# Optimization experiments

Hardware: AMD Instinct MI355X
Metric: run time of the kernel (lower is better)

Reference implementation:

```python
import jax, jax.numpy as jnp
import numpy as np

H = 8       # heads
D = 512     # hidden_size
DH = D // H # head dim
FF = 2048   # hardcoded FFN hidden in source


def _layernorm(x, g, b, eps=1e-5):
    mu = jnp.mean(x, axis=-1, keepdims=True)
    var = jnp.var(x, axis=-1, keepdims=True)
    return (x - mu) * jax.lax.rsqrt(var + eps) * g + b


def setup_inputs() -> dict:
    key = jax.random.key(0)
    ks = jax.random.split(key, 12)
    B, S = 2, 4096
    s = lambda fan_in: 1.0 / np.sqrt(fan_in)
    return {
        "reaction": jax.random.normal(ks[0], (B, S, D), dtype=jnp.float32),
        "mask": jnp.ones((B, 1, 1, S), dtype=jnp.int32),
        # attention weights stored as [in, out] (torch Linear weight.T)
        "Wq": jax.random.uniform(ks[1], (D, D), jnp.float32, -s(D), s(D)),
        "Wk": jax.random.uniform(ks[2], (D, D), jnp.float32, -s(D), s(D)),
        "Wv": jax.random.uniform(ks[3], (D, D), jnp.float32, -s(D), s(D)),
        "Wo": jax.random.uniform(ks[4], (D, D), jnp.float32, -s(D), s(D)),
        "bo": jnp.zeros((D,), jnp.float32),
        "W1": jax.random.uniform(ks[5], (D, FF), jnp.float32, -s(D), s(D)),
        "b1": jnp.zeros((FF,), jnp.float32),
        "W2": jax.random.uniform(ks[6], (FF, D), jnp.float32, -s(FF), s(FF)),
        "b2": jnp.zeros((D,), jnp.float32),
        "g_sa": jnp.ones((D,), jnp.float32),
        "b_sa": jnp.zeros((D,), jnp.float32),
        "g_ff": jnp.ones((D,), jnp.float32),
        "b_ff": jnp.zeros((D,), jnp.float32),
    }


def reference(reaction, mask, Wq, Wk, Wv, Wo, bo, W1, b1, W2, b2, g_sa, b_sa, g_ff, b_ff):
    B, S, _ = reaction.shape
    # --- self-attention part (pre-norm) ---
    x = _layernorm(reaction, g_sa, b_sa)
    q = (x @ Wq).reshape(B, S, H, DH)
    k = (x @ Wk).reshape(B, S, H, DH)
    v = (x @ Wv).reshape(B, S, H, DH)
    scale = DH ** (-0.5)
    scores = jnp.einsum('bqhd,bkhd->bhqk', q * scale, k)  # [B,H,S,S]
    scores = jnp.where(mask == 0, -jnp.inf, scores)
    att = jax.nn.softmax(scores, axis=-1)
    ctx = jnp.einsum('bhqk,bkhd->bqhd', att, v).reshape(B, S, D)
    attn_out = jax.nn.gelu(ctx @ Wo + bo, approximate=False)  # GELU after output proj (as in source)
    x = attn_out + reaction
    # --- feed-forward part (pre-norm) ---
    y = _layernorm(x, g_ff, b_ff)
    y = jax.nn.gelu(y @ W1 + b1, approximate=False) @ W2 + b2
    return y + x
```

## Files before the change

### kernel.cpp

```cpp
#include <hip/hip_runtime.h>
#include <hip/hip_bf16.h>
#include <math.h>

#define HN 8
#define DM 512
#define DHD 64
#define FFD 2048
#define BB 2
#define SS 4096
#define MT (BB*SS)

typedef __bf16 bf16_t;
typedef __bf16 bf16x8 __attribute__((ext_vector_type(8)));
typedef __bf16 bf16x4 __attribute__((ext_vector_type(4)));
typedef float  floatx4 __attribute__((ext_vector_type(4)));

__device__ __forceinline__ void async_copy16(const bf16_t* g, bf16_t* l) {
  __builtin_amdgcn_global_load_lds((const __attribute__((address_space(1))) void*)g,
                                   (__attribute__((address_space(3))) void*)l,
                                   16, 0, 0);
}

#if __has_builtin(__builtin_amdgcn_exp2f)
__device__ __forceinline__ float fast_exp2(float x) { return __builtin_amdgcn_exp2f(x); }
#else
__device__ __forceinline__ float fast_exp2(float x) { return __expf(x * 0.69314718056f); }
#endif

__device__ __forceinline__ float gelu_f(float x) {
  float y = 0.7978845608f * (x + 0.044715f * x * x * x);
  float e = fast_exp2(y * 2.885390082f);
  float th = 1.0f - 2.0f / (e + 1.0f);
  return 0.5f * x * (1.0f + th);
}

__global__ __launch_bounds__(256)
void ln_kernel(const float* __restrict__ x, const float* __restrict__ g,
               const float* __restrict__ be, bf16_t* __restrict__ out)
{
  const int wave = threadIdx.x >> 6, lane = threadIdx.x & 63;
  const int row = blockIdx.x * 4 + wave;
  const float* xr = x + (size_t)row * DM + lane * 8;
  float4 a = *(const float4*)xr;
  float4 c = *(const float4*)(xr + 4);
  float s  = (a.x + a.y) + (a.z + a.w) + (c.x + c.y) + (c.z + c.w);
  float s2 = (a.x*a.x + a.y*a.y) + (a.z*a.z + a.w*a.w)
           + (c.x*c.x + c.y*c.y) + (c.z*c.z + c.w*c.w);
#pragma unroll
  for (int o = 1; o < 64; o <<= 1) { s += __shfl_xor(s, o); s2 += __shfl_xor(s2, o); }
  const float mu = s * (1.0f / DM);
  const float rv = rsqrtf(s2 * (1.0f / DM) - mu * mu + 1e-5f);
  float4 g0 = *(const float4*)(g + lane * 8);
  float4 g1 = *(const float4*)(g + lane * 8 + 4);
  float4 b0 = *(const float4*)(be + lane * 8);
  float4 b1 = *(const float4*)(be + lane * 8 + 4);
  bf16x8 o8;
  o8[0] = (bf16_t)((a.x - mu) * rv * g0.x + b0.x);
  o8[1] = (bf16_t)((a.y - mu) * rv * g0.y + b0.y);
  o8[2] = (bf16_t)((a.z - mu) * rv * g0.z + b0.z);
  o8[3] = (bf16_t)((a.w - mu) * rv * g0.w + b0.w);
  o8[4] = (bf16_t)((c.x - mu) * rv * g1.x + b1.x);
  o8[5] = (bf16_t)((c.y - mu) * rv * g1.y + b1.y);
  o8[6] = (bf16_t)((c.z - mu) * rv * g1.z + b1.z);
  o8[7] = (bf16_t)((c.w - mu) * rv * g1.w + b1.w);
  *(bf16x8*)(out + (size_t)row * DM + lane * 8) = o8;
}

__global__ __launch_bounds__(256)
void prep_weights(const float* __restrict__ Wq, const float* __restrict__ Wk,
                  const float* __restrict__ Wv, const float* __restrict__ Wo,
                  const float* __restrict__ W1, const float* __restrict__ W2,
                  bf16_t* __restrict__ WqkvT, bf16_t* __restrict__ WoT,
                  bf16_t* __restrict__ W1T, bf16_t* __restrict__ W2T)
{
  const int bid = blockIdx.x;
  const float* src; bf16_t* dst; int Kd, Nd, n0, k0;
  if (bid < 768) {
    int seg = bid >> 8, t = bid & 255;
    src = (seg == 0) ? Wq : (seg == 1) ? Wk : Wv;
    dst = WqkvT + (size_t)seg * 512 * 512;
    Kd = 512; Nd = 512; n0 = (t & 15) * 32; k0 = (t >> 4) * 32;
  } else if (bid < 1024) {
    int t = bid - 768; src = Wo; dst = WoT;
    Kd = 512; Nd = 512; n0 = (t & 15) * 32; k0 = (t >> 4) * 32;
  } else if (bid < 2048) {
    int t = bid - 1024; src = W1; dst = W1T;
    Kd = 512; Nd = 2048; n0 = (t & 63) * 32; k0 = (t >> 6) * 32;
  } else {
    int t = bid - 2048; src = W2; dst = W2T;
    Kd = 2048; Nd = 512; n0 = (t & 15) * 32; k0 = (t >> 4) * 32;
  }
  __shared__ float tile[32][33];
  const int tx = threadIdx.x & 31, ty = threadIdx.x >> 5;
#pragma unroll
  for (int i = 0; i < 32; i += 8)
    tile[ty + i][tx] = src[(size_t)(k0 + ty + i) * Nd + n0 + tx];
  __syncthreads();
#pragma unroll
  for (int i = 0; i < 32; i += 8)
    dst[(size_t)(n0 + ty + i) * Kd + k0 + tx] = (bf16_t)tile[tx][ty + i];
}

template <int MI, int NJ, int EPI>
__global__ __launch_bounds__(256)
void gemm_bt(const bf16_t* __restrict__ A, const bf16_t* __restrict__ Bt,
             const int M, const int N, const int K,
             const float* __restrict__ bias, const float* __restrict__ res,
             bf16_t* __restrict__ outb, float* __restrict__ outf,
             bf16_t* __restrict__ out2, bf16_t* __restrict__ out3, const int ldt)
{
  constexpr int MTILE = 32 * MI, NTILE = 32 * NJ;
  constexpr int ACOPY = MTILE / 32;
  constexpr int BCOPY = NTILE / 32;
  __shared__ __align__(16) bf16_t lA[MTILE * 64];
  __shared__ __align__(16) bf16_t lB[NTILE * 64];
  const int tid = threadIdx.x;
  const int wave = tid >> 6, lane = tid & 63;
  const int wm = wave & 1, wn = wave >> 1;
  const int quad = lane >> 4, l16 = lane & 15;

  int srA[ACOPY > BCOPY ? ACOPY : BCOPY], scA[ACOPY > BCOPY ? ACOPY : BCOPY];
#pragma unroll
  for (int i = 0; i < (ACOPY > BCOPY ? ACOPY : BCOPY); ++i) {
    int flat = tid + 256 * i;
    int r = flat >> 3, ch = flat & 7;
    srA[i] = r;
    scA[i] = (ch ^ (r & 7)) * 8;
  }
  const bf16_t* Ab = A + (size_t)(blockIdx.x * MTILE) * K;
  const bf16_t* Bb = Bt + (size_t)(blockIdx.y * NTILE) * K;

  const floatx4 vzero = {0.f, 0.f, 0.f, 0.f};
  floatx4 acc[MI][NJ];
#pragma unroll
  for (int i = 0; i < MI; ++i)
#pragma unroll
    for (int j = 0; j < NJ; ++j) acc[i][j] = vzero;

  for (int k0 = 0; k0 < K; k0 += 64) {
    __syncthreads();
#pragma unroll
    for (int i = 0; i < ACOPY; ++i)
      async_copy16(Ab + (size_t)srA[i] * K + k0 + scA[i], lA + (tid + 256 * i) * 8);
#pragma unroll
    for (int i = 0; i < BCOPY; ++i)
      async_copy16(Bb + (size_t)srA[i] * K + k0 + scA[i], lB + (tid + 256 * i) * 8);
    __syncthreads();
#pragma unroll
    for (int c = 0; c < 2; ++c) {
      bf16x8 af[MI], bfv[NJ];
#pragma unroll
      for (int i = 0; i < MI; ++i)
        af[i] = *(const bf16x8*)(lA + (wm * 16 * MI + i * 16 + l16) * 64
                                 + (((c * 4 + quad) ^ (l16 & 7)) * 8));
#pragma unroll
      for (int j = 0; j < NJ; ++j)
        bfv[j] = *(const bf16x8*)(lB + (wn * 16 * NJ + j * 16 + l16) * 64
                                  + (((c * 4 + quad) ^ (l16 & 7)) * 8));
#pragma unroll
      for (int i = 0; i < MI; ++i)
#pragma unroll
        for (int j = 0; j < NJ; ++j)
          acc[i][j] = __builtin_amdgcn_mfma_f32_16x16x32_bf16(af[i], bfv[j], acc[i][j], 0, 0, 0);
    }
  }

  const int m00 = blockIdx.x * MTILE + wm * 16 * MI;
  const int n00 = blockIdx.y * NTILE + wn * 16 * NJ;
#pragma unroll
  for (int i = 0; i < MI; ++i) {
#pragma unroll
    for (int j = 0; j < NJ; ++j) {
      const int m0 = m00 + i * 16 + quad * 4;
      const int n  = n00 + j * 16 + l16;
      floatx4 v = acc[i][j];
      if (EPI == 2) {
        const float bb = bias[n];
#pragma unroll
        for (int r = 0; r < 4; ++r)
          outf[(size_t)(m0 + r) * N + n] = gelu_f(v[r] + bb) + res[(size_t)(m0 + r) * N + n];
      } else if (EPI == 3) {
        const float bb = bias[n];
#pragma unroll
        for (int r = 0; r < 4; ++r)
          outb[(size_t)(m0 + r) * N + n] = (bf16_t)gelu_f(v[r] + bb);
      } else if (EPI == 4) {
        const float bb = bias[n];
#pragma unroll
        for (int r = 0; r < 4; ++r)
          outf[(size_t)(m0 + r) * N + n] = v[r] + bb + res[(size_t)(m0 + r) * N + n];
      } else {
        const int seg = blockIdx.y >> 2;
        if (seg == 0) {
#pragma unroll
          for (int r = 0; r < 4; ++r)
            outb[(size_t)(m0 + r) * 512 + n] = (bf16_t)(v[r] * 0.180336879f);
        } else if (seg == 1) {
#pragma unroll
          for (int r = 0; r < 4; ++r) out2[(size_t)(m0 + r) * 512 + (n - 512)] = (bf16_t)v[r];
        } else {
          const int o = m0 & 31;
          const int p0 = (m0 & ~31) + ((o >> 2) & 3) * 8 + ((o >> 4) << 2);
          bf16x4 pk = {(bf16_t)v[0], (bf16_t)v[1], (bf16_t)v[2], (bf16_t)v[3]};
          *(bf16x4*)(out3 + (size_t)(n - 1024) * ldt + p0) = pk;
        }
      }
    }
  }
}

__global__ __launch_bounds__(256, 2)
void attn_kernel(const bf16_t* __restrict__ qm, const bf16_t* __restrict__ km,
                 const bf16_t* __restrict__ vtm, const int* __restrict__ mask,
                 bf16_t* __restrict__ ctx)
{
  const int flat = blockIdx.x + 32 * (blockIdx.y + 8 * blockIdx.z);
  const int swz = (flat & 7) * 64 + (flat >> 3);
  const int b = swz >> 8, h = (swz >> 5) & 7;
  const int q0 = (swz & 31) * 128;
  const int tid = threadIdx.x;
  const int wave = tid >> 6, lane = tid & 63;
  const int quad = lane >> 4, l16 = lane & 15;

  __shared__ __align__(16) bf16_t lK[2][128 * DHD];
  __shared__ __align__(16) bf16_t lV[2][DHD * 128];
  __shared__ int sclean[4];

  const int* maskb = mask + b * SS;

  unsigned um = 0xFFFFFFFFu;
#pragma unroll
  for (int i = 0; i < 4; ++i) {
    int4 m = *(const int4*)(maskb + tid * 16 + i * 4);
    um = min(um, min(min((unsigned)m.x, (unsigned)m.y), min((unsigned)m.z, (unsigned)m.w)));
  }
#pragma unroll
  for (int o = 1; o < 64; o <<= 1) um = min(um, (unsigned)__shfl_xor((int)um, o));
  if (lane == 0) sclean[wave] = (int)um;
  __syncthreads();
  const bool clean = (min(min((unsigned)sclean[0], (unsigned)sclean[1]),
                          min((unsigned)sclean[2], (unsigned)sclean[3])) != 0u);

  const size_t qrow0 = (size_t)b * SS + q0;
  bf16x8 qa[2][2];
#pragma unroll
  for (int mb = 0; mb < 2; ++mb)
#pragma unroll
    for (int cc = 0; cc < 2; ++cc)
      qa[mb][cc] = *(const bf16x8*)(qm + (qrow0 + wave * 32 + mb * 16 + l16) * DM
                                    + h * DHD + cc * 32 + quad * 8);

  const floatx4 vzero = {0.f, 0.f, 0.f, 0.f};
  floatx4 cacc[2][4];
  float lsum[2] = {0.f, 0.f};
#pragma unroll
  for (int mb = 0; mb < 2; ++mb)
#pragma unroll
    for (int nb = 0; nb < 4; ++nb) cacc[mb][nb] = vzero;

  const bf16_t* Kb = km + (size_t)b * SS * DM + h * DHD;
  const bf16_t* Vb = vtm + (size_t)(h * DHD) * MT + (size_t)b * SS;

  const bf16_t* pk[4]; const bf16_t* pv[4];
#pragma unroll
  for (int i = 0; i < 4; ++i) {
    int p = tid + 256 * i;
    int key = p >> 3, cs = (p & 7) ^ (key & 7);
    pk[i] = Kb + (size_t)key * DM + cs * 8;
    int dh = p >> 4, cs2 = (p & 15) ^ (dh & 7);
    pv[i] = Vb + (size_t)dh * MT + cs2 * 8;
  }

  auto stage = [&](int buf, int s0) {
#pragma unroll
    for (int i = 0; i < 4; ++i) {
      int p8 = (tid + 256 * i) * 8;
      async_copy16(pk[i] + (size_t)s0 * DM, lK[buf] + p8);
      async_copy16(pv[i] + s0, lV[buf] + p8);
    }
  };

  auto compute = [&](const bf16_t* __restrict__ lKb, const bf16_t* __restrict__ lVb,
                     int s0) {
#pragma unroll
    for (int c = 0; c < 4; ++c) {
      floatx4 sa[2], sb[2];
      sa[0] = vzero; sa[1] = vzero; sb[0] = vzero; sb[1] = vzero;
#pragma unroll
      for (int cc = 0; cc < 2; ++cc) {
        const int ko = ((cc * 4 + quad) ^ (l16 & 7)) * 8;
        bf16x8 kf0 = *(const bf16x8*)(lKb + (c * 32 + l16) * 64 + ko);
        bf16x8 kf1 = *(const bf16x8*)(lKb + (c * 32 + 16 + l16) * 64 + ko);
        __builtin_amdgcn_s_setprio(1);
#pragma unroll
        for (int mb = 0; mb < 2; ++mb) {
          sa[mb] = __builtin_amdgcn_mfma_f32_16x16x32_bf16(kf0, qa[mb][cc], sa[mb], 0, 0, 0);
          sb[mb] = __builtin_amdgcn_mfma_f32_16x16x32_bf16(kf1, qa[mb][cc], sb[mb], 0, 0, 0);
        }
        __builtin_amdgcn_s_setprio(0);
      }

      if (!clean) {
        const int4 m0 = *(const int4*)(maskb + s0 + c * 32 + quad * 4);
        const int4 m1 = *(const int4*)(maskb + s0 + c * 32 + 16 + quad * 4);
#pragma unroll
        for (int mb = 0; mb < 2; ++mb) {
          if (m0.x == 0) sa[mb][0] = -1e30f;
          if (m0.y == 0) sa[mb][1] = -1e30f;
          if (m0.z == 0) sa[mb][2] = -1e30f;
          if (m0.w == 0) sa[mb][3] = -1e30f;
          if (m1.x == 0) sb[mb][0] = -1e30f;
          if (m1.y == 0) sb[mb][1] = -1e30f;
          if (m1.z == 0) sb[mb][2] = -1e30f;
          if (m1.w == 0) sb[mb][3] = -1e30f;
        }
      }

      bf16x8 pf[2];
#pragma unroll
      for (int mb = 0; mb < 2; ++mb) {
        float e0 = fast_exp2(sa[mb][0]), e1 = fast_exp2(sa[mb][1]);
        float e2 = fast_exp2(sa[mb][2]), e3 = fast_exp2(sa[mb][3]);
        float e4 = fast_exp2(sb[mb][0]), e5 = fast_exp2(sb[mb][1]);
        float e6 = fast_exp2(sb[mb][2]), e7 = fast_exp2(sb[mb][3]);
        lsum[mb] += ((e0 + e1) + (e2 + e3)) + ((e4 + e5) + (e6 + e7));
        pf[mb][0] = (bf16_t)e0; pf[mb][1] = (bf16_t)e1;
        pf[mb][2] = (bf16_t)e2; pf[mb][3] = (bf16_t)e3;
        pf[mb][4] = (bf16_t)e4; pf[mb][5] = (bf16_t)e5;
        pf[mb][6] = (bf16_t)e6; pf[mb][7] = (bf16_t)e7;
      }
      const int ch = (c * 4 + quad) ^ (l16 & 7);
      __builtin_amdgcn_s_setprio(1);
#pragma unroll
      for (int nb = 0; nb < 4; ++nb) {
        bf16x8 av = *(const bf16x8*)(lVb + (nb * 16 + l16) * 128 + ch * 8);
        cacc[0][nb] = __builtin_amdgcn_mfma_f32_16x16x32_bf16(av, pf[0], cacc[0][nb], 0, 0, 0);
        cacc[1][nb] = __builtin_amdgcn_mfma_f32_16x16x32_bf16(av, pf[1], cacc[1][nb], 0, 0, 0);
      }
      __builtin_amdgcn_s_setprio(0);
    }
  };

  stage(0, 0);
#pragma unroll 1
  for (int s0 = 0; s0 < SS; s0 += 256) {
    __syncthreads();
    stage(1, s0 + 128);
    compute(lK[0], lV[0], s0);
    __syncthreads();
    if (s0 + 256 < SS) stage(0, s0 + 256);
    compute(lK[1], lV[1], s0 + 128);
  }

#pragma unroll
  for (int mb = 0; mb < 2; ++mb) {
    float tot = lsum[mb];
    tot += __shfl_xor(tot, 16);
    tot += __shfl_xor(tot, 32);
    const float inv = 1.0f / tot;
    const size_t qrow = qrow0 + wave * 32 + mb * 16 + l16;
#pragma unroll
    for (int nb = 0; nb < 4; ++nb) {
      bf16x4 o = {(bf16_t)(cacc[mb][nb][0] * inv), (bf16_t)(cacc[mb][nb][1] * inv),
                  (bf16_t)(cacc[mb][nb][2] * inv), (bf16_t)(cacc[mb][nb][3] * inv)};
      *(bf16x4*)(ctx + qrow * DM + h * DHD + nb * 16 + quad * 4) = o;
    }
  }
}

extern "C" void kernel_launch(void* const* d_in, const int* in_sizes, int n_in,
                              void* d_out, int out_size, void* d_ws, size_t ws_size,
                              hipStream_t stream)
{
  (void)in_sizes; (void)n_in; (void)out_size; (void)ws_size;
  const float* reaction = (const float*)d_in[0];
  const int*   mask     = (const int*)d_in[1];
  const float* Wq = (const float*)d_in[2];
  const float* Wk = (const float*)d_in[3];
  const float* Wv = (const float*)d_in[4];
  const float* Wo = (const float*)d_in[5];
  const float* bo = (const float*)d_in[6];
  const float* W1 = (const float*)d_in[7];
  const float* b1 = (const float*)d_in[8];
  const float* W2 = (const float*)d_in[9];
  const float* b2 = (const float*)d_in[10];
  const float* g_sa = (const float*)d_in[11];
  const float* b_sa = (const float*)d_in[12];
  const float* g_ff = (const float*)d_in[13];
  const float* b_ff = (const float*)d_in[14];
  float* out = (float*)d_out;

  char* ws = (char*)d_ws;
  size_t off = 0;
  auto take = [&](size_t bytes) -> char* {
    char* p = ws + off;
    off += (bytes + 255) & ~(size_t)255;
    return p;
  };

  bf16_t* xln   = (bf16_t*)take((size_t)MT * DM * 2);
  bf16_t* WqkvT = (bf16_t*)take((size_t)3 * DM * DM * 2);
  bf16_t* WoT   = (bf16_t*)take((size_t)DM * DM * 2);
  bf16_t* W1T   = (bf16_t*)take((size_t)FFD * DM * 2);
  bf16_t* W2T   = (bf16_t*)take((size_t)DM * FFD * 2);
  bf16_t* qb    = (bf16_t*)take((size_t)MT * DM * 2);
  bf16_t* kb    = (bf16_t*)take((size_t)MT * DM * 2);
  bf16_t* vtb   = (bf16_t*)take((size_t)DM * MT * 2);
  bf16_t* ctx   = (bf16_t*)take((size_t)MT * DM * 2);
  float*  x2    = (float*)take((size_t)MT * DM * 4);
  bf16_t* yb    = xln;
  bf16_t* hb    = qb;

  ln_kernel<<<MT / 4, 256, 0, stream>>>(reaction, g_sa, b_sa, xln);
  prep_weights<<<3072, 256, 0, stream>>>(Wq, Wk, Wv, Wo, W1, W2, WqkvT, WoT, W1T, W2T);

  gemm_bt<4, 4, 5><<<dim3(64, 12), 256, 0, stream>>>(xln, WqkvT, MT, 3 * DM, DM,
                                                     nullptr, nullptr, qb, nullptr, kb, vtb, MT);

  attn_kernel<<<dim3(SS / 128, HN, BB), 256, 0, stream>>>(qb, kb, vtb, mask, ctx);

  gemm_bt<4, 2, 2><<<dim3(64, 8), 256, 0, stream>>>(ctx, WoT, MT, DM, DM,
                                                    bo, reaction, nullptr, x2, nullptr, nullptr, 0);

  ln_kernel<<<MT / 4, 256, 0, stream>>>(x2, g_ff, b_ff, yb);
  gemm_bt<4, 4, 3><<<dim3(64, 16), 256, 0, stream>>>(yb, W1T, MT, FFD, DM,
                                                     b1, nullptr, hb, nullptr, nullptr, nullptr, 0);
  gemm_bt<4, 2, 4><<<dim3(64, 8), 256, 0, stream>>>(hb, W2T, MT, DM, FFD,
                                                    b2, x2, nullptr, out, nullptr, nullptr, 0);
}
```

Measured before the change: 271.1 us.

## Halve attention query tile and key block to raise occupancy

The attention kernel now gives each block 64 query rows (16 per wave) instead of 128, and streams K/V in 64-key chunks instead of 128. This doubles the grid to 1024 blocks, halves shared memory per block and raises the launch-bounds occupancy target from 2 to 4 blocks per CU. The cost is that each K/V tile loaded into LDS is reused by half as many query rows, which doubles total K/V traffic and the number of barriers per key processed.

```diff
diff --git a/kernel.cpp b/kernel.cpp
--- a/kernel.cpp
+++ b/kernel.cpp
@@ -209,21 +209,21 @@
   }
 }
 
-__global__ __launch_bounds__(256, 2)
+__global__ __launch_bounds__(256, 4)
 void attn_kernel(const bf16_t* __restrict__ qm, const bf16_t* __restrict__ km,
                  const bf16_t* __restrict__ vtm, const int* __restrict__ mask,
                  bf16_t* __restrict__ ctx)
 {
-  const int flat = blockIdx.x + 32 * (blockIdx.y + 8 * blockIdx.z);
-  const int swz = (flat & 7) * 64 + (flat >> 3);
-  const int b = swz >> 8, h = (swz >> 5) & 7;
-  const int q0 = (swz & 31) * 128;
+  const int flat = blockIdx.x + 64 * (blockIdx.y + 8 * blockIdx.z);
+  const int swz = (flat & 7) * 128 + (flat >> 3);
+  const int b = swz >> 9, h = (swz >> 6) & 7;
+  const int q0 = (swz & 63) * 64;
   const int tid = threadIdx.x;
   const int wave = tid >> 6, lane = tid & 63;
   const int quad = lane >> 4, l16 = lane & 15;
 
-  __shared__ __align__(16) bf16_t lK[2][128 * DHD];
-  __shared__ __align__(16) bf16_t lV[2][DHD * 128];
+  __shared__ __align__(16) bf16_t lK[2][64 * DHD];
+  __shared__ __align__(16) bf16_t lV[2][DHD * 64];
   __shared__ int sclean[4];
 
   const int* maskb = mask + b * SS;
@@ -242,38 +242,34 @@
                           min((unsigned)sclean[2], (unsigned)sclean[3])) != 0u);
 
   const size_t qrow0 = (size_t)b * SS + q0;
-  bf16x8 qa[2][2];
-#pragma unroll
-  for (int mb = 0; mb < 2; ++mb)
-#pragma unroll
-    for (int cc = 0; cc < 2; ++cc)
-      qa[mb][cc] = *(const bf16x8*)(qm + (qrow0 + wave * 32 + mb * 16 + l16) * DM
-                                    + h * DHD + cc * 32 + quad * 8);
+  bf16x8 qa[2];
+#pragma unroll
+  for (int cc = 0; cc < 2; ++cc)
+    qa[cc] = *(const bf16x8*)(qm + (qrow0 + wave * 16 + l16) * DM
+                              + h * DHD + cc * 32 + quad * 8);
 
   const floatx4 vzero = {0.f, 0.f, 0.f, 0.f};
-  floatx4 cacc[2][4];
-  float lsum[2] = {0.f, 0.f};
-#pragma unroll
-  for (int mb = 0; mb < 2; ++mb)
-#pragma unroll
-    for (int nb = 0; nb < 4; ++nb) cacc[mb][nb] = vzero;
+  floatx4 cacc[4];
+  float lsum = 0.f;
+#pragma unroll
+  for (int nb = 0; nb < 4; ++nb) cacc[nb] = vzero;
 
   const bf16_t* Kb = km + (size_t)b * SS * DM + h * DHD;
   const bf16_t* Vb = vtm + (size_t)(h * DHD) * MT + (size_t)b * SS;
 
-  const bf16_t* pk[4]; const bf16_t* pv[4];
-#pragma unroll
-  for (int i = 0; i < 4; ++i) {
+  const bf16_t* pk[2]; const bf16_t* pv[2];
+#pragma unroll
+  for (int i = 0; i < 2; ++i) {
     int p = tid + 256 * i;
     int key = p >> 3, cs = (p & 7) ^ (key & 7);
     pk[i] = Kb + (size_t)key * DM + cs * 8;
-    int dh = p >> 4, cs2 = (p & 15) ^ (dh & 7);
+    int dh = p >> 3, cs2 = (p & 7) ^ (dh & 7);
     pv[i] = Vb + (size_t)dh * MT + cs2 * 8;
   }
 
   auto stage = [&](int buf, int s0) {
 #pragma unroll
-    for (int i = 0; i < 4; ++i) {
+    for (int i = 0; i < 2; ++i) {
       int p8 = (tid + 256 * i) * 8;
       async_copy16(pk[i] + (size_t)s0 * DM, lK[buf] + p8);
       async_copy16(pv[i] + s0, lV[buf] + p8);
@@ -283,59 +279,49 @@
   auto compute = [&](const bf16_t* __restrict__ lKb, const bf16_t* __restrict__ lVb,
                      int s0) {
 #pragma unroll
-    for (int c = 0; c < 4; ++c) {
-      floatx4 sa[2], sb[2];
-      sa[0] = vzero; sa[1] = vzero; sb[0] = vzero; sb[1] = vzero;
+    for (int c = 0; c < 2; ++c) {
+      floatx4 sa = vzero, sb = vzero;
 #pragma unroll
       for (int cc = 0; cc < 2; ++cc) {
         const int ko = ((cc * 4 + quad) ^ (l16 & 7)) * 8;
         bf16x8 kf0 = *(const bf16x8*)(lKb + (c * 32 + l16) * 64 + ko);
         bf16x8 kf1 = *(const bf16x8*)(lKb + (c * 32 + 16 + l16) * 64 + ko);
         __builtin_amdgcn_s_setprio(1);
-#pragma unroll
-        for (int mb = 0; mb < 2; ++mb) {
-          sa[mb] = __builtin_amdgcn_mfma_f32_16x16x32_bf16(kf0, qa[mb][cc], sa[mb], 0, 0, 0);
-          sb[mb] = __builtin_amdgcn_mfma_f32_16x16x32_bf16(kf1, qa[mb][cc], sb[mb], 0, 0, 0);
-        }
+        sa = __builtin_amdgcn_mfma_f32_16x16x32_bf16(kf0, qa[cc], sa, 0, 0, 0);
+        sb = __builtin_amdgcn_mfma_f32_16x16x32_bf16(kf1, qa[cc], sb, 0, 0, 0);
         __builtin_amdgcn_s_setprio(0);
       }
 
       if (!clean) {
         const int4 m0 = *(const int4*)(maskb + s0 + c * 32 + quad * 4);
         const int4 m1 = *(const int4*)(maskb + s0 + c * 32 + 16 + quad * 4);
-#pragma unroll
-        for (int mb = 0; mb < 2; ++mb) {
-          if (m0.x == 0) sa[mb][0] = -1e30f;
-          if (m0.y == 0) sa[mb][1] = -1e30f;
-          if (m0.z == 0) sa[mb][2] = -1e30f;
-          if (m0.w == 0) sa[mb][3] = -1e30f;
-          if (m1.x == 0) sb[mb][0] = -1e30f;
-          if (m1.y == 0) sb[mb][1] = -1e30f;
-          if (m1.z == 0) sb[mb][2] = -1e30f;
-          if (m1.w == 0) sb[mb][3] = -1e30f;
-        }
+        if (m0.x == 0) sa[0] = -1e30f;
+        if (m0.y == 0) sa[1] = -1e30f;
+        if (m0.z == 0) sa[2] = -1e30f;
+        if (m0.w == 0) sa[3] = -1e30f;
+        if (m1.x == 0) sb[0] = -1e30f;
+        if (m1.y == 0) sb[1] = -1e30f;
+        if (m1.z == 0) sb[2] = -1e30f;
+        if (m1.w == 0) sb[3] = -1e30f;
       }
 
-      bf16x8 pf[2];
-#pragma unroll
-      for (int mb = 0; mb < 2; ++mb) {
-        float e0 = fast_exp2(sa[mb][0]), e1 = fast_exp2(sa[mb][1]);
-        float e2 = fast_exp2(sa[mb][2]), e3 = fast_exp2(sa[mb][3]);
-        float e4 = fast_exp2(sb[mb][0]), e5 = fast_exp2(sb[mb][1]);
-        float e6 = fast_exp2(sb[mb][2]), e7 = fast_exp2(sb[mb][3]);
-        lsum[mb] += ((e0 + e1) + (e2 + e3)) + ((e4 + e5) + (e6 + e7));
-        pf[mb][0] = (bf16_t)e0; pf[mb][1] = (bf16_t)e1;
-        pf[mb][2] = (bf16_t)e2; pf[mb][3] = (bf16_t)e3;
-        pf[mb][4] = (bf16_t)e4; pf[mb][5] = (bf16_t)e5;
-        pf[mb][6] = (bf16_t)e6; pf[mb][7] = (bf16_t)e7;
-      }
+      float e0 = fast_exp2(sa[0]), e1 = fast_exp2(sa[1]);
+      float e2 = fast_exp2(sa[2]), e3 = fast_exp2(sa[3]);
+      float e4 = fast_exp2(sb[0]), e5 = fast_exp2(sb[1]);
+      float e6 = fast_exp2(sb[2]), e7 = fast_exp2(sb[3]);
+      lsum += ((e0 + e1) + (e2 + e3)) + ((e4 + e5) + (e6 + e7));
+      bf16x8 pf;
+      pf[0] = (bf16_t)e0; pf[1] = (bf16_t)e1;
+      pf[2] = (bf16_t)e2; pf[3] = (bf16_t)e3;
+      pf[4] = (bf16_t)e4; pf[5] = (bf16_t)e5;
+      pf[6] = (bf16_t)e6; pf[7] = (bf16_t)e7;
+
       const int ch = (c * 4 + quad) ^ (l16 & 7);
       __builtin_amdgcn_s_setprio(1);
 #pragma unroll
       for (int nb = 0; nb < 4; ++nb) {
-        bf16x8 av = *(const bf16x8*)(lVb + (nb * 16 + l16) * 128 + ch * 8);
-        cacc[0][nb] = __builtin_amdgcn_mfma_f32_16x16x32_bf16(av, pf[0], cacc[0][nb], 0, 0, 0);
-        cacc[1][nb] = __builtin_amdgcn_mfma_f32_16x16x32_bf16(av, pf[1], cacc[1][nb], 0, 0, 0);
+        bf16x8 av = *(const bf16x8*)(lVb + (nb * 16 + l16) * 64 + ch * 8);
+        cacc[nb] = __builtin_amdgcn_mfma_f32_16x16x32_bf16(av, pf, cacc[nb], 0, 0, 0);
       }
       __builtin_amdgcn_s_setprio(0);
     }
@@ -343,28 +329,25 @@
 
   stage(0, 0);
 #pragma unroll 1
-  for (int s0 = 0; s0 < SS; s0 += 256) {
+  for (int s0 = 0; s0 < SS; s0 += 128) {
     __syncthreads();
-    stage(1, s0 + 128);
+    stage(1, s0 + 64);
     compute(lK[0], lV[0], s0);
     __syncthreads();
-    if (s0 + 256 < SS) stage(0, s0 + 256);
-    compute(lK[1], lV[1], s0 + 128);
-  }
-
-#pragma unroll
-  for (int mb = 0; mb < 2; ++mb) {
-    float tot = lsum[mb];
-    tot += __shfl_xor(tot, 16);
-    tot += __shfl_xor(tot, 32);
-    const float inv = 1.0f / tot;
-    const size_t qrow = qrow0 + wave * 32 + mb * 16 + l16;
-#pragma unroll
-    for (int nb = 0; nb < 4; ++nb) {
-      bf16x4 o = {(bf16_t)(cacc[mb][nb][0] * inv), (bf16_t)(cacc[mb][nb][1] * inv),
-                  (bf16_t)(cacc[mb][nb][2] * inv), (bf16_t)(cacc[mb][nb][3] * inv)};
-      *(bf16x4*)(ctx + qrow * DM + h * DHD + nb * 16 + quad * 4) = o;
-    }
+    if (s0 + 128 < SS) stage(0, s0 + 128);
+    compute(lK[1], lV[1], s0 + 64);
+  }
+
+  float tot = lsum;
+  tot += __shfl_xor(tot, 16);
+  tot += __shfl_xor(tot, 32);
+  const float inv = 1.0f / tot;
+  const size_t qrow = qrow0 + wave * 16 + l16;
+#pragma unroll
+  for (int nb = 0; nb < 4; ++nb) {
+    bf16x4 o = {(bf16_t)(cacc[nb][0] * inv), (bf16_t)(cacc[nb][1] * inv),
+                (bf16_t)(cacc[nb][2] * inv), (bf16_t)(cacc[nb][3] * inv)};
+    *(bf16x4*)(ctx + qrow * DM + h * DHD + nb * 16 + quad * 4) = o;
   }
 }
 
@@ -417,7 +400,7 @@
   gemm_bt<4, 4, 5><<<dim3(64, 12), 256, 0, stream>>>(xln, WqkvT, MT, 3 * DM, DM,
                                                      nullptr, nullptr, qb, nullptr, kb, vtb, MT);
 
-  attn_kernel<<<dim3(SS / 128, HN, BB), 256, 0, stream>>>(qb, kb, vtb, mask, ctx);
+  attn_kernel<<<dim3(SS / 64, HN, BB), 256, 0, stream>>>(qb, kb, vtb, mask, ctx);
 
   gemm_bt<4, 2, 2><<<dim3(64, 8), 256, 0, stream>>>(ctx, WoT, MT, DM, DM,
                                                     bo, reaction, nullptr, x2, nullptr, nullptr, 0);
```

Measured after the change: 286.3 us. 1.06x slower.

## Double-buffer GEMM LDS tiles in half-K stages to overlap loads with MFMA

Applied to the files above, without the earlier changes.

Splits each 64-wide K step of the bf16 GEMM into two 32-wide stages held in two LDS buffers. The async global-to-LDS copy of the next stage is issued before the MFMA work on the current stage, so load latency can overlap compute. The LDS footprint stays the same, and the swizzle pattern changes to fit 32-element rows. The catch is that there are now two barriers per 32-K half instead of per 64-K step, and whether the async loads complete before the barrier depends on the implicit waitcnt.

```diff
diff --git a/kernel.cpp b/kernel.cpp
--- a/kernel.cpp
+++ b/kernel.cpp
@@ -110,22 +110,28 @@
              bf16_t* __restrict__ out2, bf16_t* __restrict__ out3, const int ldt)
 {
   constexpr int MTILE = 32 * MI, NTILE = 32 * NJ;
-  constexpr int ACOPY = MTILE / 32;
-  constexpr int BCOPY = NTILE / 32;
-  __shared__ __align__(16) bf16_t lA[MTILE * 64];
-  __shared__ __align__(16) bf16_t lB[NTILE * 64];
+  constexpr int ACOPY = MTILE / 64;
+  constexpr int BCOPY = NTILE / 64;
+  __shared__ __align__(16) bf16_t lA[2][MTILE * 32];
+  __shared__ __align__(16) bf16_t lB[2][NTILE * 32];
   const int tid = threadIdx.x;
   const int wave = tid >> 6, lane = tid & 63;
   const int wm = wave & 1, wn = wave >> 1;
   const int quad = lane >> 4, l16 = lane & 15;
 
-  int srA[ACOPY > BCOPY ? ACOPY : BCOPY], scA[ACOPY > BCOPY ? ACOPY : BCOPY];
-#pragma unroll
-  for (int i = 0; i < (ACOPY > BCOPY ? ACOPY : BCOPY); ++i) {
-    int flat = tid + 256 * i;
-    int r = flat >> 3, ch = flat & 7;
-    srA[i] = r;
-    scA[i] = (ch ^ (r & 7)) * 8;
+  int arow[ACOPY], acol[ACOPY];
+#pragma unroll
+  for (int i = 0; i < ACOPY; ++i) {
+    int f = tid + 256 * i;
+    arow[i] = f >> 2;
+    acol[i] = ((f & 3) ^ ((f >> 3) & 3)) * 8;
+  }
+  int brow[BCOPY], bcol[BCOPY];
+#pragma unroll
+  for (int i = 0; i < BCOPY; ++i) {
+    int f = tid + 256 * i;
+    brow[i] = f >> 2;
+    bcol[i] = ((f & 3) ^ ((f >> 3) & 3)) * 8;
   }
   const bf16_t* Ab = A + (size_t)(blockIdx.x * MTILE) * K;
   const bf16_t* Bb = Bt + (size_t)(blockIdx.y * NTILE) * K;
@@ -137,32 +143,40 @@
 #pragma unroll
     for (int j = 0; j < NJ; ++j) acc[i][j] = vzero;
 
+  auto stage = [&](int buf, int k0) {
+#pragma unroll
+    for (int i = 0; i < ACOPY; ++i)
+      async_copy16(Ab + (size_t)arow[i] * K + k0 + acol[i], lA[buf] + (tid + 256 * i) * 8);
+#pragma unroll
+    for (int i = 0; i < BCOPY; ++i)
+      async_copy16(Bb + (size_t)brow[i] * K + k0 + bcol[i], lB[buf] + (tid + 256 * i) * 8);
+  };
+
+  const int rchunk = (quad ^ ((l16 >> 1) & 3)) * 8;
+  auto compute = [&](int buf) {
+    bf16x8 af[MI], bfv[NJ];
+#pragma unroll
+    for (int i = 0; i < MI; ++i)
+      af[i] = *(const bf16x8*)(lA[buf] + (wm * 16 * MI + i * 16 + l16) * 32 + rchunk);
+#pragma unroll
+    for (int j = 0; j < NJ; ++j)
+      bfv[j] = *(const bf16x8*)(lB[buf] + (wn * 16 * NJ + j * 16 + l16) * 32 + rchunk);
+#pragma unroll
+    for (int i = 0; i < MI; ++i)
+#pragma unroll
+      for (int j = 0; j < NJ; ++j)
+        acc[i][j] = __builtin_amdgcn_mfma_f32_16x16x32_bf16(af[i], bfv[j], acc[i][j], 0, 0, 0);
+  };
+
+  stage(0, 0);
+#pragma unroll 1
   for (int k0 = 0; k0 < K; k0 += 64) {
     __syncthreads();
-#pragma unroll
-    for (int i = 0; i < ACOPY; ++i)
-      async_copy16(Ab + (size_t)srA[i] * K + k0 + scA[i], lA + (tid + 256 * i) * 8);
-#pragma unroll
-    for (int i = 0; i < BCOPY; ++i)
-      async_copy16(Bb + (size_t)srA[i] * K + k0 + scA[i], lB + (tid + 256 * i) * 8);
+    stage(1, k0 + 32);
+    compute(0);
     __syncthreads();
-#pragma unroll
-    for (int c = 0; c < 2; ++c) {
-      bf16x8 af[MI], bfv[NJ];
-#pragma unroll
-      for (int i = 0; i < MI; ++i)
-        af[i] = *(const bf16x8*)(lA + (wm * 16 * MI + i * 16 + l16) * 64
-                                 + (((c * 4 + quad) ^ (l16 & 7)) * 8));
-#pragma unroll
-      for (int j = 0; j < NJ; ++j)
-        bfv[j] = *(const bf16x8*)(lB + (wn * 16 * NJ + j * 16 + l16) * 64
-                                  + (((c * 4 + quad) ^ (l16 & 7)) * 8));
-#pragma unroll
-      for (int i = 0; i < MI; ++i)
-#pragma unroll
-        for (int j = 0; j < NJ; ++j)
-          acc[i][j] = __builtin_amdgcn_mfma_f32_16x16x32_bf16(af[i], bfv[j], acc[i][j], 0, 0, 0);
-    }
+    if (k0 + 64 < K) stage(0, k0 + 64);
+    compute(1);
   }
 
   const int m00 = blockIdx.x * MTILE + wm * 16 * MI;
```

Result: slower. 287.0 us (+5.8%).

## Split attention waves across query and key halves with LDS reduction

Applied to the files above, without the earlier changes.

Reassigns the four waves of the attention kernel so each pair covers 64 query rows and each wave handles half of every 128-key tile, instead of each wave owning 32 query rows across all keys. K and V fragments are loaded from LDS once per tile and reused across four query sub-blocks, cutting LDS read traffic per MFMA. Partial outputs and softmax denominators from the two key-half waves are combined through shared memory at the end. In exchange, register pressure rises (more accumulators and Q fragments held), which may hurt occupancy under the 2-blocks-per-SM launch bound, and an extra reduction step is added.

```diff
diff --git a/kernel.cpp b/kernel.cpp
--- a/kernel.cpp
+++ b/kernel.cpp
@@ -221,10 +221,13 @@
   const int tid = threadIdx.x;
   const int wave = tid >> 6, lane = tid & 63;
   const int quad = lane >> 4, l16 = lane & 15;
-
-  __shared__ __align__(16) bf16_t lK[2][128 * DHD];
-  __shared__ __align__(16) bf16_t lV[2][DHD * 128];
+  const int qhalf = wave >> 1, khalf = wave & 1;
+
+  __shared__ __align__(16) bf16_t smem[4 * 128 * DHD];
+  __shared__ float sden[2][4][16];
   __shared__ int sclean[4];
+  bf16_t* const lK = smem;
+  bf16_t* const lV = smem + 2 * 128 * DHD;
 
   const int* maskb = mask + b * SS;
 
@@ -242,19 +245,19 @@
                           min((unsigned)sclean[2], (unsigned)sclean[3])) != 0u);
 
   const size_t qrow0 = (size_t)b * SS + q0;
-  bf16x8 qa[2][2];
-#pragma unroll
-  for (int mb = 0; mb < 2; ++mb)
+  bf16x8 qa[4][2];
+#pragma unroll
+  for (int mb = 0; mb < 4; ++mb)
 #pragma unroll
     for (int cc = 0; cc < 2; ++cc)
-      qa[mb][cc] = *(const bf16x8*)(qm + (qrow0 + wave * 32 + mb * 16 + l16) * DM
+      qa[mb][cc] = *(const bf16x8*)(qm + (qrow0 + qhalf * 64 + mb * 16 + l16) * DM
                                     + h * DHD + cc * 32 + quad * 8);
 
   const floatx4 vzero = {0.f, 0.f, 0.f, 0.f};
-  floatx4 cacc[2][4];
-  float lsum[2] = {0.f, 0.f};
-#pragma unroll
-  for (int mb = 0; mb < 2; ++mb)
+  floatx4 cacc[4][4];
+  float lsum[4] = {0.f, 0.f, 0.f, 0.f};
+#pragma unroll
+  for (int mb = 0; mb < 4; ++mb)
 #pragma unroll
     for (int nb = 0; nb < 4; ++nb) cacc[mb][nb] = vzero;
 
@@ -275,68 +278,69 @@
 #pragma unroll
     for (int i = 0; i < 4; ++i) {
       int p8 = (tid + 256 * i) * 8;
-      async_copy16(pk[i] + (size_t)s0 * DM, lK[buf] + p8);
-      async_copy16(pv[i] + s0, lV[buf] + p8);
+      async_copy16(pk[i] + (size_t)s0 * DM, lK + buf * 128 * DHD + p8);
+      async_copy16(pv[i] + s0, lV + buf * DHD * 128 + p8);
     }
   };
 
-  auto compute = [&](const bf16_t* __restrict__ lKb, const bf16_t* __restrict__ lVb,
-                     int s0) {
-#pragma unroll
-    for (int c = 0; c < 4; ++c) {
-      floatx4 sa[2], sb[2];
-      sa[0] = vzero; sa[1] = vzero; sb[0] = vzero; sb[1] = vzero;
-#pragma unroll
-      for (int cc = 0; cc < 2; ++cc) {
-        const int ko = ((cc * 4 + quad) ^ (l16 & 7)) * 8;
-        bf16x8 kf0 = *(const bf16x8*)(lKb + (c * 32 + l16) * 64 + ko);
-        bf16x8 kf1 = *(const bf16x8*)(lKb + (c * 32 + 16 + l16) * 64 + ko);
-        __builtin_amdgcn_s_setprio(1);
-#pragma unroll
-        for (int mb = 0; mb < 2; ++mb) {
-          sa[mb] = __builtin_amdgcn_mfma_f32_16x16x32_bf16(kf0, qa[mb][cc], sa[mb], 0, 0, 0);
-          sb[mb] = __builtin_amdgcn_mfma_f32_16x16x32_bf16(kf1, qa[mb][cc], sb[mb], 0, 0, 0);
-        }
-        __builtin_amdgcn_s_setprio(0);
+  auto compute = [&](int buf, int s0) {
+    const bf16_t* lKb = lK + buf * 128 * DHD;
+    const bf16_t* lVb = lV + buf * DHD * 128;
+    bf16x8 kf[4][2], av[2][4];
+#pragma unroll
+    for (int kk = 0; kk < 4; ++kk)
+#pragma unroll
+      for (int cc = 0; cc < 2; ++cc)
+        kf[kk][cc] = *(const bf16x8*)(lKb + (khalf * 64 + kk * 16 + l16) * 64
+                                      + (((cc * 4 + quad) ^ (l16 & 7)) * 8));
+#pragma unroll
+    for (int c2 = 0; c2 < 2; ++c2)
+#pragma unroll
+      for (int nb = 0; nb < 4; ++nb)
+        av[c2][nb] = *(const bf16x8*)(lVb + (nb * 16 + l16) * 128
+                                      + ((((khalf * 2 + c2) * 4 + quad) ^ (l16 & 7)) * 8));
+
+#pragma unroll
+    for (int mb = 0; mb < 4; ++mb) {
+      floatx4 s4[4];
+#pragma unroll
+      for (int kk = 0; kk < 4; ++kk) s4[kk] = vzero;
+      __builtin_amdgcn_s_setprio(1);
+#pragma unroll
+      for (int kk = 0; kk < 4; ++kk) {
+        s4[kk] = __builtin_amdgcn_mfma_f32_16x16x32_bf16(kf[kk][0], qa[mb][0], s4[kk], 0, 0, 0);
+        s4[kk] = __builtin_amdgcn_mfma_f32_16x16x32_bf16(kf[kk][1], qa[mb][1], s4[kk], 0, 0, 0);
       }
+      __builtin_amdgcn_s_setprio(0);
 
       if (!clean) {
-        const int4 m0 = *(const int4*)(maskb + s0 + c * 32 + quad * 4);
-        const int4 m1 = *(const int4*)(maskb + s0 + c * 32 + 16 + quad * 4);
-#pragma unroll
-        for (int mb = 0; mb < 2; ++mb) {
-          if (m0.x == 0) sa[mb][0] = -1e30f;
-          if (m0.y == 0) sa[mb][1] = -1e30f;
-          if (m0.z == 0) sa[mb][2] = -1e30f;
-          if (m0.w == 0) sa[mb][3] = -1e30f;
-          if (m1.x == 0) sb[mb][0] = -1e30f;
-          if (m1.y == 0) sb[mb][1] = -1e30f;
-          if (m1.z == 0) sb[mb][2] = -1e30f;
-          if (m1.w == 0) sb[mb][3] = -1e30f;
+#pragma unroll
+        for (int kk = 0; kk < 4; ++kk) {
+          const int4 m0 = *(const int4*)(maskb + s0 + khalf * 64 + kk * 16 + quad * 4);
+          if (m0.x == 0) s4[kk][0] = -1e30f;
+          if (m0.y == 0) s4[kk][1] = -1e30f;
+          if (m0.z == 0) s4[kk][2] = -1e30f;
+          if (m0.w == 0) s4[kk][3] = -1e30f;
         }
       }
 
       bf16x8 pf[2];
 #pragma unroll
-      for (int mb = 0; mb < 2; ++mb) {
-        float e0 = fast_exp2(sa[mb][0]), e1 = fast_exp2(sa[mb][1]);
-        float e2 = fast_exp2(sa[mb][2]), e3 = fast_exp2(sa[mb][3]);
-        float e4 = fast_exp2(sb[mb][0]), e5 = fast_exp2(sb[mb][1]);
-        float e6 = fast_exp2(sb[mb][2]), e7 = fast_exp2(sb[mb][3]);
-        lsum[mb] += ((e0 + e1) + (e2 + e3)) + ((e4 + e5) + (e6 + e7));
-        pf[mb][0] = (bf16_t)e0; pf[mb][1] = (bf16_t)e1;
-        pf[mb][2] = (bf16_t)e2; pf[mb][3] = (bf16_t)e3;
-        pf[mb][4] = (bf16_t)e4; pf[mb][5] = (bf16_t)e5;
-        pf[mb][6] = (bf16_t)e6; pf[mb][7] = (bf16_t)e7;
+      for (int kk = 0; kk < 4; ++kk) {
+        float e0 = fast_exp2(s4[kk][0]), e1 = fast_exp2(s4[kk][1]);
+        float e2 = fast_exp2(s4[kk][2]), e3 = fast_exp2(s4[kk][3]);
+        lsum[mb] += (e0 + e1) + (e2 + e3);
+        const int hi = (kk & 1) * 4;
+        pf[kk >> 1][hi + 0] = (bf16_t)e0; pf[kk >> 1][hi + 1] = (bf16_t)e1;
+        pf[kk >> 1][hi + 2] = (bf16_t)e2; pf[kk >> 1][hi + 3] = (bf16_t)e3;
       }
-      const int ch = (c * 4 + quad) ^ (l16 & 7);
       __builtin_amdgcn_s_setprio(1);
 #pragma unroll
-      for (int nb = 0; nb < 4; ++nb) {
-        bf16x8 av = *(const bf16x8*)(lVb + (nb * 16 + l16) * 128 + ch * 8);
-        cacc[0][nb] = __builtin_amdgcn_mfma_f32_16x16x32_bf16(av, pf[0], cacc[0][nb], 0, 0, 0);
-        cacc[1][nb] = __builtin_amdgcn_mfma_f32_16x16x32_bf16(av, pf[1], cacc[1][nb], 0, 0, 0);
-      }
+      for (int c2 = 0; c2 < 2; ++c2)
+#pragma unroll
+        for (int nb = 0; nb < 4; ++nb)
+          cacc[mb][nb] = __builtin_amdgcn_mfma_f32_16x16x32_bf16(av[c2][nb], pf[c2],
+                                                                 cacc[mb][nb], 0, 0, 0);
       __builtin_amdgcn_s_setprio(0);
     }
   };
@@ -346,24 +350,48 @@
   for (int s0 = 0; s0 < SS; s0 += 256) {
     __syncthreads();
     stage(1, s0 + 128);
-    compute(lK[0], lV[0], s0);
+    compute(0, s0);
     __syncthreads();
     if (s0 + 256 < SS) stage(0, s0 + 256);
-    compute(lK[1], lV[1], s0 + 128);
-  }
-
-#pragma unroll
-  for (int mb = 0; mb < 2; ++mb) {
-    float tot = lsum[mb];
-    tot += __shfl_xor(tot, 16);
-    tot += __shfl_xor(tot, 32);
-    const float inv = 1.0f / tot;
-    const size_t qrow = qrow0 + wave * 32 + mb * 16 + l16;
-#pragma unroll
-    for (int nb = 0; nb < 4; ++nb) {
-      bf16x4 o = {(bf16_t)(cacc[mb][nb][0] * inv), (bf16_t)(cacc[mb][nb][1] * inv),
-                  (bf16_t)(cacc[mb][nb][2] * inv), (bf16_t)(cacc[mb][nb][3] * inv)};
-      *(bf16x4*)(ctx + qrow * DM + h * DHD + nb * 16 + quad * 4) = o;
+    compute(1, s0 + 128);
+  }
+
+#pragma unroll
+  for (int mb = 0; mb < 4; ++mb) {
+    float t = lsum[mb];
+    t += __shfl_xor(t, 16);
+    t += __shfl_xor(t, 32);
+    lsum[mb] = t;
+  }
+  __syncthreads();
+  float* const sO = (float*)smem;
+  if (khalf == 0) {
+    if (lane < 16) {
+#pragma unroll
+      for (int mb = 0; mb < 4; ++mb) sden[qhalf][mb][l16] = lsum[mb];
+    }
+    float* base = sO + qhalf * (64 * 68);
+#pragma unroll
+    for (int mb = 0; mb < 4; ++mb)
+#pragma unroll
+      for (int nb = 0; nb < 4; ++nb)
+        *(floatx4*)(base + (mb * 16 + l16) * 68 + nb * 16 + quad * 4) = cacc[mb][nb];
+  }
+  __syncthreads();
+  if (khalf == 1) {
+    const float* base = sO + qhalf * (64 * 68);
+#pragma unroll
+    for (int mb = 0; mb < 4; ++mb) {
+      const float inv = 1.0f / (sden[qhalf][mb][l16] + lsum[mb]);
+      const size_t qrow = qrow0 + qhalf * 64 + mb * 16 + l16;
+#pragma unroll
+      for (int nb = 0; nb < 4; ++nb) {
+        floatx4 o4 = *(const floatx4*)(base + (mb * 16 + l16) * 68 + nb * 16 + quad * 4);
+        o4 += cacc[mb][nb];
+        bf16x4 o = {(bf16_t)(o4[0] * inv), (bf16_t)(o4[1] * inv),
+                    (bf16_t)(o4[2] * inv), (bf16_t)(o4[3] * inv)};
+        *(bf16x4*)(ctx + qrow * DM + h * DHD + nb * 16 + quad * 4) = o;
+      }
     }
   }
 }
```

After: 436.6 us. 61.0% more time.
